# Performance work log

Hardware: AMD Instinct MI355X
Metric: run time of the kernel (lower is better)

## Reference

```python
import jax, jax.numpy as jnp
import numpy as np

D = 1024        # embedding_dim
N = 200000      # number of train embeddings
C = 50          # n_concepts
B = 4096        # batch size
NUM_CLASSES = 4
TOPK = 50


def setup_inputs() -> dict:
    key = jax.random.key(0)
    k1, k2, k3, k4, k5 = jax.random.split(key, 5)
    return {
        "concept": jax.random.normal(k1, (D, C), dtype=jnp.float32),
        "train_embeddings": jax.random.normal(k2, (D, N), dtype=jnp.float32),
        "train_embedding": jax.random.normal(k3, (B, D), dtype=jnp.float32),
        "hx_weight": jax.random.normal(k4, (NUM_CLASSES, D), dtype=jnp.float32) * 0.02,
        "hx_bias": jax.random.normal(k5, (NUM_CLASSES,), dtype=jnp.float32) * 0.02,
        "topk": TOPK,
    }


def reference(concept, train_embeddings, train_embedding, hx_weight, hx_bias, topk):
    n_concepts = concept.shape[1]
    k = int(topk)

    # projection of inputs onto concept subspace: P = C (C^T C)^{-1} C^T
    gram = concept.T @ concept                      # (C, C)
    proj_matrix = concept @ jnp.linalg.inv(gram) @ concept.T   # (D, D)
    proj = proj_matrix @ train_embedding.T          # (D, B)
    y_pred = proj.T @ hx_weight.T + hx_bias         # (B, num_classes)
    orig_pred = train_embedding @ hx_weight.T + hx_bias

    # batched KNN: squared euclidean distance of every concept to every train embedding
    # (sqrt is monotone, ordering identical to torch.norm-based distances)
    te_sq = jnp.sum(train_embeddings * train_embeddings, axis=0)   # (N,)
    c_sq = jnp.sum(concept * concept, axis=0)                      # (C,)
    dots = concept.T @ train_embeddings                            # (C, N)
    dist2 = c_sq[:, None] + te_sq[None, :] - 2.0 * dots            # (C, N)
    _, knn_idx = jax.lax.top_k(-dist2, k)                          # (C, k) smallest distances

    # gather neighbor activations: (D, C, k)
    knn_act = jnp.take(train_embeddings, knn_idx.reshape(-1), axis=1).reshape(
        train_embeddings.shape[0], n_concepts, k)

    # L_sparse_1 = mean_c [ sum_{d,k} concept[d,c]*knn[d,c,k] / k ]
    L_sparse_1 = jnp.einsum("dc,dck->", concept, knn_act) / (k * n_concepts)

    eye = jnp.eye(n_concepts, dtype=concept.dtype)
    mask = 1.0 - eye
    L_sparse_2 = jnp.mean(gram * mask)
    norm_metrics = jnp.mean(gram * eye)
    similarity_penalty = jnp.mean(jnp.abs(gram - eye))

    return (orig_pred, y_pred, L_sparse_1, L_sparse_2, norm_metrics, similarity_penalty)
```

## Files before the change

### kernel.cpp

```cpp
#include <hip/hip_runtime.h>
#include <stdint.h>

#define D 1024
#define N 200000
#define C 50
#define B 4096
#define CLS 4
#define KParts 16
#define CAP 4096
#define BN 256
#define NBLK 782
#define NSLOT (NBLK * 8)
#define BLROW 260

typedef __attribute__((ext_vector_type(8))) short short8;
typedef __attribute__((ext_vector_type(4))) float f32x4;

static const size_t OFF_U     = 0;
static const size_t OFF_TESQ  = (size_t)C * N;
static const size_t OFF_GPART = OFF_TESQ + N;
static const size_t OFF_WPART = OFF_GPART + KParts * 2500;
static const size_t OFF_ABF   = ((OFF_WPART + KParts * 200 + 3) / 4) * 4;
static const size_t OFF_RANGE = OFF_ABF + 32768;
static const size_t OFF_SUMS  = OFF_RANGE + 2 * NSLOT;
static const size_t OFF_CNT   = OFF_SUMS + C;
static const size_t OFF_W8    = ((OFF_CNT + 1 + 3) / 4) * 4;

__device__ __forceinline__ unsigned mapf(float v) {
    unsigned u = __float_as_uint(v);
    return (u & 0x80000000u) ? ~u : (u | 0x80000000u);
}
__device__ __forceinline__ float unmapf(unsigned u) {
    unsigned b = (u & 0x80000000u) ? (u ^ 0x80000000u) : ~u;
    return __uint_as_float(b);
}
__device__ __forceinline__ unsigned keyu(float dot, float tesq) {
    return mapf(fmaf(-2.0f, dot, tesq));
}
__device__ __forceinline__ unsigned short f2bf(float f) {
    unsigned u = __float_as_uint(f);
    u += 0x7FFFu + ((u >> 16) & 1u);
    return (unsigned short)(u >> 16);
}
__device__ __forceinline__ float bf2f(unsigned short h) {
    return __uint_as_float((unsigned)h << 16);
}

__global__ __launch_bounds__(256) void kprep(
    const float* __restrict__ concept, const float* __restrict__ hxw,
    float* __restrict__ ws)
{
    int t = threadIdx.x;

    if (blockIdx.x < KParts) {
        __shared__ __align__(16) float ct[64 * 50];
        __shared__ float hs[4 * 64];
        int bid = blockIdx.x;
        int d0 = bid * 64;

        for (int i = t; i < 64 * 50; i += 256) ct[i] = concept[d0 * 50 + i];
        {
            int j = t >> 6, dd = t & 63;
            hs[t] = hxw[j * D + d0 + dd];
        }
        __syncthreads();

        float* gp = ws + OFF_GPART + (size_t)bid * 2500;
        for (int p = t; p < 2500; p += 256) {
            int i = p / 50, j = p - i * 50;
            float acc = 0.f;
            #pragma unroll 8
            for (int dd = 0; dd < 64; ++dd)
                acc = fmaf(ct[dd * 50 + i], ct[dd * 50 + j], acc);
            gp[p] = acc;
        }
        float* wp = ws + OFF_WPART + (size_t)bid * 200;
        if (t < 200) {
            int j = t / 50, c = t - j * 50;
            float acc = 0.f;
            #pragma unroll 8
            for (int dd = 0; dd < 64; ++dd)
                acc = fmaf(hs[j * 64 + dd], ct[dd * 50 + c], acc);
            wp[t] = acc;
        }
        return;
    }

    unsigned short* ap = (unsigned short*)(ws + OFF_ABF);
    for (int idx = t; idx < 8192; idx += 256) {
        int ks = idx >> 8;
        int g  = (idx >> 6) & 3;
        int m  = idx & 63;
        unsigned short v[8];
        #pragma unroll
        for (int j = 0; j < 8; ++j) {
            int k = ks * 32 + g * 8 + j;
            v[j] = (m < 50) ? f2bf(concept[k * 50 + m]) : (unsigned short)0;
        }
        uint4 pk;
        pk.x = (unsigned)v[0] | ((unsigned)v[1] << 16);
        pk.y = (unsigned)v[2] | ((unsigned)v[3] << 16);
        pk.z = (unsigned)v[4] | ((unsigned)v[5] << 16);
        pk.w = (unsigned)v[6] | ((unsigned)v[7] << 16);
        *(uint4*)(ap + (size_t)idx * 8) = pk;
    }
}

__global__ __launch_bounds__(512, 4) void kgemm(
    const float* __restrict__ concept, const float* __restrict__ te,
    const float* __restrict__ hxw, float* __restrict__ ws,
    float* __restrict__ out)
{
    __shared__ __align__(16) unsigned char smem[42496];

    int t = threadIdx.x;
    int l = t & 63, w = t >> 6;

    if (blockIdx.x == NBLK) {
        float* gsh  = (float*)smem;
        float* Asv  = (float*)(smem + 10000);
        float* colp = (float*)(smem + 21200);
        float* part = (float*)(smem + 21408);

        if (t == 0) ((unsigned*)(ws + OFF_CNT))[0] = 0u;

        float s_all = 0.f, s_tr = 0.f, s_abs = 0.f;
        for (int p = t; p < 2500; p += 512) {
            float g = 0.f;
            #pragma unroll
            for (int b = 0; b < KParts; ++b)
                g += ws[OFF_GPART + (size_t)b * 2500 + p];
            gsh[p] = g;
            int i = p / 50, jj = p - i * 50;
            float e = (i == jj) ? 1.0f : 0.0f;
            s_all += g;
            if (i == jj) s_tr += g;
            s_abs += fabsf(g - e);
        }
        #pragma unroll
        for (int off = 32; off > 0; off >>= 1) {
            s_all += __shfl_down(s_all, off, 64);
            s_tr  += __shfl_down(s_tr,  off, 64);
            s_abs += __shfl_down(s_abs, off, 64);
        }
        if (l == 0) { part[0 * 8 + w] = s_all; part[1 * 8 + w] = s_tr; part[2 * 8 + w] = s_abs; }
        __syncthreads();
        if (t == 0) {
            float a = 0.f, tr = 0.f, ab = 0.f;
            for (int i = 0; i < 8; ++i) {
                a += part[0 * 8 + i]; tr += part[1 * 8 + i]; ab += part[2 * 8 + i];
            }
            out[32769] = (a - tr) / 2500.0f;
            out[32770] = tr / 2500.0f;
            out[32771] = ab / 2500.0f;
        }

        for (int p = t; p < 50 * 56; p += 512) {
            int r = p / 56, col = p - r * 56;
            float v = 0.f;
            if (col < 50) v = gsh[r * 50 + col];
            else if (col < 54) {
                float ww = 0.f;
                #pragma unroll
                for (int b = 0; b < KParts; ++b)
                    ww += ws[OFF_WPART + (size_t)b * 200 + (col - 50) * 50 + r];
                v = ww;
            }
            Asv[p] = v;
        }
        __syncthreads();

        for (int pc = 0; pc < C; ++pc) {
            if (t < C) colp[t] = Asv[t * 56 + pc];
            __syncthreads();
            float pinv = 1.0f / colp[pc];
            if (t < 56) Asv[pc * 56 + t] *= pinv;
            __syncthreads();
            for (int p = t; p < 50 * 56; p += 512) {
                int r = p / 56, col = p - r * 56;
                if (r != pc) Asv[p] = fmaf(-colp[r], Asv[pc * 56 + col], Asv[p]);
            }
            __syncthreads();
        }

        for (int d = t; d < D; d += 512) {
            float wy0 = 0.f, wy1 = 0.f, wy2 = 0.f, wy3 = 0.f;
            for (int c = 0; c < C; ++c) {
                float cv = concept[d * 50 + c];
                wy0 = fmaf(cv, Asv[c * 56 + 50], wy0);
                wy1 = fmaf(cv, Asv[c * 56 + 51], wy1);
                wy2 = fmaf(cv, Asv[c * 56 + 52], wy2);
                wy3 = fmaf(cv, Asv[c * 56 + 53], wy3);
            }
            float4 lo, hi;
            lo.x = hxw[0 * D + d]; lo.y = hxw[1 * D + d];
            lo.z = hxw[2 * D + d]; lo.w = hxw[3 * D + d];
            hi.x = wy0; hi.y = wy1; hi.z = wy2; hi.w = wy3;
            *(float4*)(ws + OFF_W8 + (size_t)d * 8)     = lo;
            *(float4*)(ws + OFF_W8 + (size_t)d * 8 + 4) = hi;
        }
        return;
    }

    unsigned* Blb = (unsigned*)smem;
    float* tsp = (float*)(smem + 33280);
    float* tsf = (float*)(smem + 33280 + 8192);

    int nbase = blockIdx.x * BN;
    int nq = t & 63, rp = w;
    int ncol0 = nbase + nq * 4;
    bool colv = (ncol0 < N);

    f32x4 accf[2][4];
    #pragma unroll
    for (int mf = 0; mf < 2; ++mf)
        #pragma unroll
        for (int nf = 0; nf < 4; ++nf)
            accf[mf][nf] = (f32x4)(0.0f);
    float ts0 = 0.f, ts1 = 0.f, ts2 = 0.f, ts3 = 0.f;

    const unsigned short* ap = (const unsigned short*)(ws + OFF_ABF);
    int g = l >> 4;
    int mhalf = w >> 2;
    int nnb = (w & 3) * 64 + (l & 15);

    auto cvt_write = [&](int buf, float4* xr) {
        #pragma unroll
        for (int pi = 0; pi < 2; ++pi) {
            int pair = rp + pi * 8;
            float4 xa = xr[2 * pi], xb = xr[2 * pi + 1];
            unsigned short a0 = f2bf(xa.x), a1 = f2bf(xa.y), a2 = f2bf(xa.z), a3 = f2bf(xa.w);
            unsigned short b0 = f2bf(xb.x), b1 = f2bf(xb.y), b2 = f2bf(xb.z), b3 = f2bf(xb.w);
            float fa0 = bf2f(a0), fa1 = bf2f(a1), fa2 = bf2f(a2), fa3 = bf2f(a3);
            float fb0 = bf2f(b0), fb1 = bf2f(b1), fb2 = bf2f(b2), fb3 = bf2f(b3);
            ts0 = fmaf(fa0, fa0, fmaf(fb0, fb0, ts0));
            ts1 = fmaf(fa1, fa1, fmaf(fb1, fb1, ts1));
            ts2 = fmaf(fa2, fa2, fmaf(fb2, fb2, ts2));
            ts3 = fmaf(fa3, fa3, fmaf(fb3, fb3, ts3));
            uint4 pk;
            pk.x = (unsigned)a0 | ((unsigned)b0 << 16);
            pk.y = (unsigned)a1 | ((unsigned)b1 << 16);
            pk.z = (unsigned)a2 | ((unsigned)b2 << 16);
            pk.w = (unsigned)a3 | ((unsigned)b3 << 16);
            *(uint4*)(&Blb[buf * (16 * BLROW) + pair * BLROW + nq * 4]) = pk;
        }
    };
    auto ldtile = [&](int ks, float4* xr) {
        #pragma unroll
        for (int pi = 0; pi < 2; ++pi) {
            int pair = rp + pi * 8;
            int k0 = ks * 32 + pair * 2;
            if (colv) {
                xr[2 * pi]     = *(const float4*)(te + (size_t)k0 * N + ncol0);
                xr[2 * pi + 1] = *(const float4*)(te + (size_t)(k0 + 1) * N + ncol0);
            } else {
                xr[2 * pi]     = make_float4(0.f, 0.f, 0.f, 0.f);
                xr[2 * pi + 1] = make_float4(0.f, 0.f, 0.f, 0.f);
            }
        }
    };

    {
        float4 xr[4];
        ldtile(0, xr);
        cvt_write(0, xr);
    }

    #pragma unroll 1
    for (int ks = 0; ks < 32; ++ks) {
        __syncthreads();
        float4 nx[4];
        if (ks < 31) ldtile(ks + 1, nx);

        short8 af0 = *(const short8*)(ap + ((size_t)(ks * 4 + g) * 64 + mhalf * 32 + 0 * 16 + (l & 15)) * 8);
        short8 af1 = *(const short8*)(ap + ((size_t)(ks * 4 + g) * 64 + mhalf * 32 + 1 * 16 + (l & 15)) * 8);

        const unsigned* Bc = Blb + (ks & 1) * (16 * BLROW);
        #pragma unroll
        for (int nf = 0; nf < 4; ++nf) {
            int nn = nnb + nf * 16;
            union { unsigned u[4]; short8 s; } bu;
            bu.u[0] = Bc[(g * 4 + 0) * BLROW + nn];
            bu.u[1] = Bc[(g * 4 + 1) * BLROW + nn];
            bu.u[2] = Bc[(g * 4 + 2) * BLROW + nn];
            bu.u[3] = Bc[(g * 4 + 3) * BLROW + nn];
            accf[0][nf] = __builtin_amdgcn_mfma_f32_16x16x32_bf16(af0, bu.s, accf[0][nf], 0, 0, 0);
            accf[1][nf] = __builtin_amdgcn_mfma_f32_16x16x32_bf16(af1, bu.s, accf[1][nf], 0, 0, 0);
        }

        if (ks < 31) cvt_write((ks + 1) & 1, nx);
    }

    __syncthreads();
    tsp[rp * 256 + nq * 4 + 0] = ts0;
    tsp[rp * 256 + nq * 4 + 1] = ts1;
    tsp[rp * 256 + nq * 4 + 2] = ts2;
    tsp[rp * 256 + nq * 4 + 3] = ts3;
    __syncthreads();
    if (t < 64) {
        float4 s = make_float4(0.f, 0.f, 0.f, 0.f);
        #pragma unroll
        for (int r = 0; r < 8; ++r) {
            float4 v = *(const float4*)(&tsp[r * 256 + t * 4]);
            s.x += v.x; s.y += v.y; s.z += v.z; s.w += v.w;
        }
        *(float4*)(&tsf[t * 4]) = s;
        if (nbase + t * 4 < N)
            *(float4*)(ws + OFF_TESQ + nbase + t * 4) = s;
    }
    __syncthreads();

    unsigned* uws = (unsigned*)ws;
    unsigned kmin = 0xFFFFFFFFu, kmax = 0u;
    #pragma unroll
    for (int mf = 0; mf < 2; ++mf) {
        #pragma unroll
        for (int nf = 0; nf < 4; ++nf) {
            int nloc = nnb + nf * 16;
            int nabs = nbase + nloc;
            #pragma unroll
            for (int r = 0; r < 4; ++r) {
                int c = mhalf * 32 + mf * 16 + (l >> 4) * 4 + r;
                if (c < 50 && nabs < N) {
                    unsigned u = keyu(accf[mf][nf][r], tsf[nloc]);
                    uws[(size_t)c * N + nabs] = u;
                    kmin = min(kmin, u);
                    kmax = max(kmax, u);
                }
            }
        }
    }
    #pragma unroll
    for (int off = 32; off > 0; off >>= 1) {
        kmin = min(kmin, (unsigned)__shfl_down((int)kmin, off, 64));
        kmax = max(kmax, (unsigned)__shfl_down((int)kmax, off, 64));
    }
    if (l == 0) {
        int slot = blockIdx.x * 8 + w;
        ((unsigned*)(ws + OFF_RANGE))[2 * slot]     = kmin;
        ((unsigned*)(ws + OFF_RANGE))[2 * slot + 1] = kmax;
    }
}

__global__ __launch_bounds__(256) void kpred(
    const float* __restrict__ X, const float* __restrict__ hxb,
    const float* __restrict__ ws, float* __restrict__ out)
{
    int t = threadIdx.x;
    int lane = t & 63, w = t >> 6;
    int r = blockIdx.x * 4 + w;
    const float* xr = X + (size_t)r * D;
    const float* w8 = ws + OFF_W8;

    float acc[8];
    #pragma unroll
    for (int j = 0; j < 8; ++j) acc[j] = 0.f;
    #pragma unroll
    for (int i = 0; i < 16; ++i) {
        int d = i * 64 + lane;
        float x = xr[d];
        float4 lo = *(const float4*)(w8 + (size_t)d * 8);
        float4 hi = *(const float4*)(w8 + (size_t)d * 8 + 4);
        acc[0] = fmaf(x, lo.x, acc[0]);
        acc[1] = fmaf(x, lo.y, acc[1]);
        acc[2] = fmaf(x, lo.z, acc[2]);
        acc[3] = fmaf(x, lo.w, acc[3]);
        acc[4] = fmaf(x, hi.x, acc[4]);
        acc[5] = fmaf(x, hi.y, acc[5]);
        acc[6] = fmaf(x, hi.z, acc[6]);
        acc[7] = fmaf(x, hi.w, acc[7]);
    }
    #pragma unroll
    for (int j = 0; j < 8; ++j) {
        float v = acc[j];
        #pragma unroll
        for (int off = 32; off > 0; off >>= 1) v += __shfl_down(v, off, 64);
        if (lane == 0) {
            float b = hxb[j & 3];
            if (j < 4) out[(size_t)r * CLS + j] = v + b;
            else       out[16384 + (size_t)r * CLS + (j - 4)] = v + b;
        }
    }
}

__global__ __launch_bounds__(1024) void k4_select(
    const float* __restrict__ ws, float* __restrict__ wsw,
    float* __restrict__ out, const int* __restrict__ topk)
{
    int c = blockIdx.x, t = threadIdx.x;
    int lane = t & 63, wid = t >> 6;
    const unsigned* uarr = (const unsigned*)ws + (size_t)c * N;
    const float* tesq = ws + OFF_TESQ;

    __shared__ unsigned hist[4096];
    __shared__ unsigned wsum[16], woff[16];
    __shared__ unsigned wmn[16], wmx[16];
    __shared__ unsigned sh_ulo, sh_uhi;
    __shared__ unsigned sh_bin; __shared__ int sh_rem;
    __shared__ int cnt;
    __shared__ unsigned cand_u[CAP];
    __shared__ int      cand_i[CAP];
    __shared__ float fred[16];

    {
        const unsigned* rg = (const unsigned*)(ws + OFF_RANGE);
        unsigned mn = 0xFFFFFFFFu, mx = 0u;
        for (int i = t; i < NSLOT; i += 1024) {
            mn = min(mn, rg[2 * i]);
            mx = max(mx, rg[2 * i + 1]);
        }
        #pragma unroll
        for (int off = 32; off > 0; off >>= 1) {
            mn = min(mn, (unsigned)__shfl_down((int)mn, off, 64));
            mx = max(mx, (unsigned)__shfl_down((int)mx, off, 64));
        }
        if (lane == 0) { wmn[wid] = mn; wmx[wid] = mx; }
        __syncthreads();
        if (t == 0) {
            unsigned m0 = 0xFFFFFFFFu, m1 = 0u;
            for (int w = 0; w < 16; ++w) { m0 = min(m0, wmn[w]); m1 = max(m1, wmx[w]); }
            sh_ulo = m0; sh_uhi = m1;
        }
        __syncthreads();
    }
    unsigned ubase = sh_ulo;
    unsigned ulo = sh_ulo, uhi = sh_uhi;
    int rem = *topk;
    unsigned long long width = (unsigned long long)(uhi - ulo) + 1ull;

    for (int i = t; i < 4096; i += 1024) hist[i] = 0u;
    __syncthreads();
    for (int n = t; n < N; n += 1024) {
        unsigned u = uarr[n];
        unsigned bin = (unsigned)(((unsigned long long)(u - ubase) * 4096ull) / width);
        atomicAdd(&hist[bin], 1u);
    }
    __syncthreads();
    {
        unsigned b0 = (unsigned)t * 4u;
        unsigned h0 = hist[b0], h1 = hist[b0 + 1], h2 = hist[b0 + 2], h3 = hist[b0 + 3];
        unsigned s4 = h0 + h1 + h2 + h3;
        unsigned x = s4;
        #pragma unroll
        for (int off = 1; off < 64; off <<= 1) {
            unsigned y = (unsigned)__shfl_up((int)x, off, 64);
            if (lane >= off) x += y;
        }
        if (lane == 63) wsum[wid] = x;
        __syncthreads();
        if (t == 0) {
            unsigned run = 0;
            for (int w = 0; w < 16; ++w) { woff[w] = run; run += wsum[w]; }
        }
        __syncthreads();
        unsigned cumBefore = woff[wid] + x - s4;
        unsigned remu = (unsigned)rem;
        if (cumBefore < remu && remu <= cumBefore + s4) {
            unsigned cum = cumBefore, bin = b0, r2 = 1;
            unsigned hh[4] = {h0, h1, h2, h3};
            #pragma unroll
            for (int j = 0; j < 4; ++j) {
                if (cum + hh[j] >= remu) { bin = b0 + j; r2 = remu - cum; break; }
                cum += hh[j];
            }
            sh_bin = bin; sh_rem = (int)r2;
        }
        __syncthreads();
        unsigned b = sh_bin;
        rem = sh_rem;
        ulo = ubase + (unsigned)(((unsigned long long)b * width + 4095ull) / 4096ull);
        uhi = ubase + (unsigned)((((unsigned long long)(b + 1) * width + 4095ull) / 4096ull) - 1ull);
        __syncthreads();
    }

    if (t == 0) cnt = 0;
    __syncthreads();
    float lsum = 0.f;
    for (int n = t; n < N; n += 1024) {
        unsigned u = uarr[n];
        if (u < ulo) {
            lsum += 0.5f * (tesq[n] - unmapf(u));
        } else if (u <= uhi) {
            int s = atomicAdd(&cnt, 1);
            if (s < CAP) { cand_u[s] = u; cand_i[s] = n; }
        }
    }
    __syncthreads();
    int cc = cnt < CAP ? cnt : CAP;
    for (int ci = t; ci < cc; ci += 1024) {
        unsigned ui = cand_u[ci]; int ii = cand_i[ci];
        int rank = 0;
        for (int j = 0; j < cc; ++j) {
            unsigned uj = cand_u[j];
            rank += (uj < ui || (uj == ui && cand_i[j] < ii)) ? 1 : 0;
        }
        if (rank < rem) lsum += 0.5f * (tesq[ii] - unmapf(ui));
    }
    #pragma unroll
    for (int off = 32; off > 0; off >>= 1) lsum += __shfl_down(lsum, off, 64);
    if (lane == 0) fred[wid] = lsum;
    __syncthreads();
    if (t == 0) {
        float tot = 0.f;
        for (int w = 0; w < 16; ++w) tot += fred[w];
        wsw[OFF_SUMS + c] = tot;
        __threadfence();
        unsigned done = atomicAdd((unsigned*)(wsw + OFF_CNT), 1u);
        if (done == C - 1) {
            float s = 0.f;
            for (int i = 0; i < C; ++i) s += atomicAdd(&wsw[OFF_SUMS + i], 0.0f);
            out[32768] = s / (float)((*topk) * C);
        }
    }
}

extern "C" void kernel_launch(void* const* d_in, const int* in_sizes, int n_in,
                              void* d_out, int out_size, void* d_ws, size_t ws_size,
                              hipStream_t stream) {
    (void)in_sizes; (void)n_in; (void)out_size; (void)ws_size;
    const float* concept = (const float*)d_in[0];
    const float* te      = (const float*)d_in[1];
    const float* X       = (const float*)d_in[2];
    const float* hxw     = (const float*)d_in[3];
    const float* hxb     = (const float*)d_in[4];
    const int*   topk    = (const int*)d_in[5];
    float* out = (float*)d_out;
    float* ws  = (float*)d_ws;

    kprep<<<dim3(KParts + 1), dim3(256), 0, stream>>>(concept, hxw, ws);
    kgemm<<<dim3(NBLK + 1), dim3(512), 0, stream>>>(concept, te, hxw, ws, out);
    kpred<<<dim3(B / 4), dim3(256), 0, stream>>>(X, hxb, ws, out);
    k4_select<<<dim3(C), dim3(1024), 0, stream>>>(ws, ws, out, topk);
}
```

Measured before the change: 509.0 us.

## Deepen global-load prefetch to two tiles and use lighter tile barriers

The main distance GEMM loop now prefetches train-embedding tiles two k-steps ahead, using two register buffers in a manually unrolled-by-two loop, instead of one step ahead. This is meant to hide more global memory latency behind the MFMA work. __syncthreads is replaced by a custom barrier that waits only on LDS counters (lgkmcnt) so outstanding global loads stay in flight across the barrier. The bf16 conversion now uses the packed __float22bfloat162_rn intrinsic. The extra register buffer raises register pressure, which could reduce occupancy.

Result: no change. 508.2 us, median of 2 (-0.2%).

```diff
diff --git a/kernel.cpp b/kernel.cpp
--- a/kernel.cpp
+++ b/kernel.cpp
@@ -1,4 +1,5 @@
 #include <hip/hip_runtime.h>
+#include <hip/hip_bf16.h>
 #include <stdint.h>
 
 #define D 1024
@@ -42,9 +43,12 @@
     u += 0x7FFFu + ((u >> 16) & 1u);
     return (unsigned short)(u >> 16);
 }
-__device__ __forceinline__ float bf2f(unsigned short h) {
-    return __uint_as_float((unsigned)h << 16);
-}
+
+#define TILE_BARRIER() do {                                   \
+    asm volatile("s_waitcnt lgkmcnt(0)" ::: "memory");        \
+    __builtin_amdgcn_s_barrier();                             \
+    asm volatile("" ::: "memory");                            \
+} while (0)
 
 __global__ __launch_bounds__(256) void kprep(
     const float* __restrict__ concept, const float* __restrict__ hxw,
@@ -224,27 +228,6 @@
     int mhalf = w >> 2;
     int nnb = (w & 3) * 64 + (l & 15);
 
-    auto cvt_write = [&](int buf, float4* xr) {
-        #pragma unroll
-        for (int pi = 0; pi < 2; ++pi) {
-            int pair = rp + pi * 8;
-            float4 xa = xr[2 * pi], xb = xr[2 * pi + 1];
-            unsigned short a0 = f2bf(xa.x), a1 = f2bf(xa.y), a2 = f2bf(xa.z), a3 = f2bf(xa.w);
-            unsigned short b0 = f2bf(xb.x), b1 = f2bf(xb.y), b2 = f2bf(xb.z), b3 = f2bf(xb.w);
-            float fa0 = bf2f(a0), fa1 = bf2f(a1), fa2 = bf2f(a2), fa3 = bf2f(a3);
-            float fb0 = bf2f(b0), fb1 = bf2f(b1), fb2 = bf2f(b2), fb3 = bf2f(b3);
-            ts0 = fmaf(fa0, fa0, fmaf(fb0, fb0, ts0));
-            ts1 = fmaf(fa1, fa1, fmaf(fb1, fb1, ts1));
-            ts2 = fmaf(fa2, fa2, fmaf(fb2, fb2, ts2));
-            ts3 = fmaf(fa3, fa3, fmaf(fb3, fb3, ts3));
-            uint4 pk;
-            pk.x = (unsigned)a0 | ((unsigned)b0 << 16);
-            pk.y = (unsigned)a1 | ((unsigned)b1 << 16);
-            pk.z = (unsigned)a2 | ((unsigned)b2 << 16);
-            pk.w = (unsigned)a3 | ((unsigned)b3 << 16);
-            *(uint4*)(&Blb[buf * (16 * BLROW) + pair * BLROW + nq * 4]) = pk;
-        }
-    };
     auto ldtile = [&](int ks, float4* xr) {
         #pragma unroll
         for (int pi = 0; pi < 2; ++pi) {
@@ -260,17 +243,32 @@
         }
     };
 
-    {
-        float4 xr[4];
-        ldtile(0, xr);
-        cvt_write(0, xr);
-    }
-
-    #pragma unroll 1
-    for (int ks = 0; ks < 32; ++ks) {
-        __syncthreads();
-        float4 nx[4];
-        if (ks < 31) ldtile(ks + 1, nx);
+    auto cvt_write = [&](int buf, float4* xr) {
+        #pragma unroll
+        for (int pi = 0; pi < 2; ++pi) {
+            int pair = rp + pi * 8;
+            float4 xa = xr[2 * pi], xb = xr[2 * pi + 1];
+            union { __hip_bfloat162 h; unsigned u; } p0, p1, p2, p3;
+            p0.h = __float22bfloat162_rn(make_float2(xa.x, xb.x));
+            p1.h = __float22bfloat162_rn(make_float2(xa.y, xb.y));
+            p2.h = __float22bfloat162_rn(make_float2(xa.z, xb.z));
+            p3.h = __float22bfloat162_rn(make_float2(xa.w, xb.w));
+            float fa0 = __uint_as_float(p0.u << 16), fb0 = __uint_as_float(p0.u & 0xFFFF0000u);
+            float fa1 = __uint_as_float(p1.u << 16), fb1 = __uint_as_float(p1.u & 0xFFFF0000u);
+            float fa2 = __uint_as_float(p2.u << 16), fb2 = __uint_as_float(p2.u & 0xFFFF0000u);
+            float fa3 = __uint_as_float(p3.u << 16), fb3 = __uint_as_float(p3.u & 0xFFFF0000u);
+            ts0 = fmaf(fa0, fa0, fmaf(fb0, fb0, ts0));
+            ts1 = fmaf(fa1, fa1, fmaf(fb1, fb1, ts1));
+            ts2 = fmaf(fa2, fa2, fmaf(fb2, fb2, ts2));
+            ts3 = fmaf(fa3, fa3, fmaf(fb3, fb3, ts3));
+            uint4 pk;
+            pk.x = p0.u; pk.y = p1.u; pk.z = p2.u; pk.w = p3.u;
+            *(uint4*)(&Blb[buf * (16 * BLROW) + pair * BLROW + nq * 4]) = pk;
+        }
+    };
+
+    auto body = [&](int ks, float4* rload, float4* rcons) {
+        if (ks < 30) ldtile(ks + 2, rload);
 
         short8 af0 = *(const short8*)(ap + ((size_t)(ks * 4 + g) * 64 + mhalf * 32 + 0 * 16 + (l & 15)) * 8);
         short8 af1 = *(const short8*)(ap + ((size_t)(ks * 4 + g) * 64 + mhalf * 32 + 1 * 16 + (l & 15)) * 8);
@@ -288,7 +286,20 @@
             accf[1][nf] = __builtin_amdgcn_mfma_f32_16x16x32_bf16(af1, bu.s, accf[1][nf], 0, 0, 0);
         }
 
-        if (ks < 31) cvt_write((ks + 1) & 1, nx);
+        if (ks < 31) cvt_write((ks + 1) & 1, rcons);
+    };
+
+    float4 r0[4], r1[4];
+    ldtile(0, r0);
+    ldtile(1, r1);
+    cvt_write(0, r0);
+
+    #pragma unroll 1
+    for (int ks = 0; ks < 32; ks += 2) {
+        TILE_BARRIER();
+        body(ks, r0, r1);
+        TILE_BARRIER();
+        body(ks + 1, r1, r0);
     }
 
     __syncthreads();
```
